# Optimization experiments

Hardware: AMD Instinct MI355X
Metric: run time of the kernel (lower is better)

## Reference

```python
import jax, jax.numpy as jnp
import numpy as np

B, T, D, H = 2, 512, 512, 8
HD = D // H
FF = 4 * D
MOM_BETA, NOV_BETA, NOV_GAIN = 0.9, 0.95, 3.0
LR_MIN, LR_MAX, MAX_FW_NORM = 0.5, 3.0, 32.0


def setup_inputs() -> dict:
    key = jax.random.key(0)
    ks = jax.random.split(key, 10)
    s = 1.0 / np.sqrt(D)
    return {
        'x': jax.random.normal(ks[0], (B, T, D), jnp.float32),
        'Wq': jax.random.normal(ks[1], (D, D), jnp.float32) * s,
        'Wk1': jax.random.normal(ks[2], (D, D), jnp.float32) * s,
        'Wk2': jax.random.normal(ks[3], (D, D), jnp.float32) * s,
        'Wv': jax.random.normal(ks[4], (D, D), jnp.float32) * s,
        'Wo': jax.random.normal(ks[5], (D, D), jnp.float32) * s,
        'lambda_logit': jnp.zeros((H,), jnp.float32),  # sigmoid -> lambda_init = 0.5
        'ln1_g': jnp.ones((D,), jnp.float32), 'ln1_b': jnp.zeros((D,), jnp.float32),
        'base_weight': jax.random.normal(ks[6], (D, D), jnp.float32) * s,  # ~xavier
        'ttt_bias': jnp.zeros((D,), jnp.float32),
        'log_inner_lr': jnp.log(jnp.asarray(0.05, jnp.float32)),
        'ln2_g': jnp.ones((D,), jnp.float32), 'ln2_b': jnp.zeros((D,), jnp.float32),
        'W1': jax.random.normal(ks[7], (FF, D), jnp.float32) * s,
        'b1': jnp.zeros((FF,), jnp.float32),
        'W2': jax.random.normal(ks[8], (D, FF), jnp.float32) * (1.0 / np.sqrt(FF)),
        'b2': jnp.zeros((D,), jnp.float32),
        'ln3_g': jnp.ones((D,), jnp.float32), 'ln3_b': jnp.zeros((D,), jnp.float32),
    }


def _ln(x, g, b):
    m = x.mean(-1, keepdims=True)
    v = jnp.mean((x - m) ** 2, -1, keepdims=True)
    return (x - m) / jnp.sqrt(v + 1e-5) * g + b


def _diff_attn(x, Wq, Wk1, Wk2, Wv, Wo, lambda_logit):
    b, t, d = x.shape
    def heads(w):
        return jnp.einsum('btd,od->bto', x, w).reshape(b, t, H, HD).transpose(0, 2, 1, 3)
    q, k1, k2, v = heads(Wq), heads(Wk1), heads(Wk2), heads(Wv)
    scale = HD ** -0.5
    s1 = jnp.einsum('bhqd,bhkd->bhqk', q, k1) * scale
    s2 = jnp.einsum('bhqd,bhkd->bhqk', q, k2) * scale
    mask = jnp.tril(jnp.ones((t, t), bool))
    neg = jnp.finfo(s1.dtype).min
    s1 = jnp.where(mask, s1, neg)
    s2 = jnp.where(mask, s2, neg)
    lam = jax.nn.sigmoid(lambda_logit)[None, :, None, None]
    attn = jax.nn.softmax(s1, -1) - lam * jax.nn.softmax(s2, -1)
    attn = attn / jnp.clip(jnp.abs(attn).sum(-1, keepdims=True), 1e-6, None)
    o = jnp.einsum('bhqk,bhkd->bhqd', attn, v).transpose(0, 2, 1, 3).reshape(b, t, d)
    return jnp.einsum('btd,od->bto', o, Wo)


def _ttt(x, base_weight, ttt_bias, log_inner_lr):
    b = x.shape[0]
    inner_lr = jnp.clip(jnp.exp(log_inner_lr), 1e-5, 1.0)
    fw0 = jnp.broadcast_to(base_weight, (b, D, D)).astype(x.dtype) + 0.0
    mom0 = jnp.zeros_like(fw0)
    ema0 = jnp.zeros((b, D), x.dtype)
    lrm0 = jnp.ones((b, 1), x.dtype)

    def step(carry, x_t):  # x_t: [B, D]
        fw, mom, ema, lrm = carry
        y = jnp.einsum('bij,bj->bi', fw, x_t) + ttt_bias
        err = (y - x_t) / float(D)  # targets=None -> target is x_t
        g = jax.lax.stop_gradient(err[:, :, None] * x_t[:, None, :])  # first_order
        mom2 = MOM_BETA * mom + (1.0 - MOM_BETA) * g
        nov = jnp.abs(x_t - ema).mean(-1, keepdims=True)  # [B, 1]
        lr_scale = jnp.clip(1.0 + NOV_GAIN * nov, LR_MIN, LR_MAX)
        lrm2 = NOV_BETA * lrm + (1.0 - NOV_BETA) * lr_scale
        ema2 = NOV_BETA * ema + (1.0 - NOV_BETA) * x_t
        fw2 = fw - (inner_lr * lrm2)[:, :, None] * mom2
        norm = jnp.clip(jnp.sqrt((fw2 * fw2).sum((1, 2), keepdims=True)), 1e-6, None)
        fw2 = fw2 * jnp.minimum(MAX_FW_NORM / norm, 1.0)
        return (fw2, mom2, ema2, lrm2), y

    _, ys = jax.lax.scan(step, (fw0, mom0, ema0, lrm0), x.transpose(1, 0, 2))
    return ys.transpose(1, 0, 2)


def reference(x, Wq, Wk1, Wk2, Wv, Wo, lambda_logit, ln1_g, ln1_b, base_weight, ttt_bias, log_inner_lr, ln2_g, ln2_b, W1, b1, W2, b2, ln3_g, ln3_b):
    h = x + _diff_attn(_ln(x, ln1_g, ln1_b), Wq, Wk1, Wk2, Wv, Wo, lambda_logit)
    h = h + _ttt(_ln(h, ln2_g, ln2_b), base_weight, ttt_bias, log_inner_lr)
    z = _ln(h, ln3_g, ln3_b)
    z = jax.nn.gelu(jnp.einsum('btd,fd->btf', z, W1) + b1, approximate=False)
    h = h + jnp.einsum('btf,df->btd', z, W2) + b2
    return h
```

## Files before the change

kernel.cpp:

```cpp
#include <hip/hip_runtime.h>
#include <hip/hip_fp16.h>

typedef _Float16 f16;
typedef f16 f16x4 __attribute__((ext_vector_type(4)));
typedef f16 f16x8 __attribute__((ext_vector_type(8)));
typedef float f32x4 __attribute__((ext_vector_type(4)));
typedef unsigned uint2v __attribute__((ext_vector_type(2)));

#define DEVI static __device__ __forceinline__

DEVI void gload_lds16(const void* g, void* l) {
  __builtin_amdgcn_global_load_lds(
      (const __attribute__((address_space(1))) unsigned int*)g,
      (__attribute__((address_space(3))) unsigned int*)l, 16, 0, 0);
}

DEVI float wave_red_sum64(float v) {
#pragma unroll
  for (int m = 1; m < 64; m <<= 1) v += __shfl_xor(v, m, 64);
  return v;
}
DEVI float wave_red_max64(float v) {
#pragma unroll
  for (int m = 1; m < 64; m <<= 1) v = fmaxf(v, __shfl_xor(v, m, 64));
  return v;
}

template <int CTRL>
DEVI float dpp_addf(float v) {
  int s = __builtin_amdgcn_update_dpp(0, __float_as_int(v), CTRL, 0xF, 0xF, true);
  return v + __int_as_float(s);
}
DEVI float xor16_add(float v) {
#if __has_builtin(__builtin_amdgcn_permlane16_swap)
  uint2v r = __builtin_amdgcn_permlane16_swap(__float_as_uint(v), __float_as_uint(v), false, false);
  return __uint_as_float(r.x) + __uint_as_float(r.y);
#else
  int s = __builtin_amdgcn_ds_swizzle(__float_as_int(v), 0x401F);
  return v + __int_as_float(s);
#endif
}
DEVI float xor32_add(float v) {
#if __has_builtin(__builtin_amdgcn_permlane32_swap)
  uint2v r = __builtin_amdgcn_permlane32_swap(__float_as_uint(v), __float_as_uint(v), false, false);
  return __uint_as_float(r.x) + __uint_as_float(r.y);
#else
  int s = __builtin_amdgcn_ds_bpermute(((threadIdx.x & 63) ^ 32) << 2, __float_as_int(v));
  return v + __int_as_float(s);
#endif
}
DEVI float allred64(float v) {
  v = dpp_addf<0xB1>(v);
  v = dpp_addf<0x4E>(v);
  v = dpp_addf<0x141>(v);
  v = dpp_addf<0x140>(v);
  v = xor16_add(v);
  return xor32_add(v);
}

__global__ void cvt_all_kernel(const float* __restrict__ s0, const float* __restrict__ s1,
                               const float* __restrict__ s2, const float* __restrict__ s3,
                               const float* __restrict__ s4, const float* __restrict__ s5,
                               const float* __restrict__ s6, f16* __restrict__ d) {
  const int blk = blockIdx.x;
  const float* s; long dofs; int local;
  if (blk < 256)       { s = s0; dofs = 0;       local = blk; }
  else if (blk < 512)  { s = s1; dofs = 262144;  local = blk - 256; }
  else if (blk < 768)  { s = s2; dofs = 524288;  local = blk - 512; }
  else if (blk < 1024) { s = s3; dofs = 786432;  local = blk - 768; }
  else if (blk < 1280) { s = s4; dofs = 1048576; local = blk - 1024; }
  else if (blk < 2304) { s = s5; dofs = 1310720; local = blk - 1280; }
  else                 { s = s6; dofs = 2359296; local = blk - 2304; }
  const long i = (long)local * 1024 + threadIdx.x * 4;
  float4 v = *(const float4*)(s + i);
  f16x4 o = {(f16)v.x, (f16)v.y, (f16)v.z, (f16)v.w};
  *(f16x4*)(d + dofs + i) = o;
}

__global__ void ln_kernel(const float* __restrict__ in, const float* __restrict__ add,
                          const float* __restrict__ g, const float* __restrict__ b,
                          float* __restrict__ sumout, float* __restrict__ lnf,
                          f16* __restrict__ lnh) {
  const int row = blockIdx.x * 4 + (threadIdx.x >> 6);
  const int lane = threadIdx.x & 63;
  const long base = (long)row * 512;
  const int c0 = lane * 4, c1 = 256 + lane * 4;
  float4 a0 = *(const float4*)(in + base + c0);
  float4 a1 = *(const float4*)(in + base + c1);
  if (add) {
    float4 d0 = *(const float4*)(add + base + c0);
    float4 d1 = *(const float4*)(add + base + c1);
    a0.x += d0.x; a0.y += d0.y; a0.z += d0.z; a0.w += d0.w;
    a1.x += d1.x; a1.y += d1.y; a1.z += d1.z; a1.w += d1.w;
  }
  if (sumout) {
    *(float4*)(sumout + base + c0) = a0;
    *(float4*)(sumout + base + c1) = a1;
  }
  float v[8] = {a0.x, a0.y, a0.z, a0.w, a1.x, a1.y, a1.z, a1.w};
  float s = 0.f;
#pragma unroll
  for (int k = 0; k < 8; k++) s += v[k];
  s = wave_red_sum64(s);
  const float mean = s * (1.f / 512.f);
  float vs = 0.f;
#pragma unroll
  for (int k = 0; k < 8; k++) { float d = v[k] - mean; vs += d * d; }
  vs = wave_red_sum64(vs);
  const float rstd = rsqrtf(vs * (1.f / 512.f) + 1e-5f);
  float4 g0 = *(const float4*)(g + c0), g1 = *(const float4*)(g + c1);
  float4 p0 = *(const float4*)(b + c0), p1 = *(const float4*)(b + c1);
  const float gg[8] = {g0.x, g0.y, g0.z, g0.w, g1.x, g1.y, g1.z, g1.w};
  const float bv[8] = {p0.x, p0.y, p0.z, p0.w, p1.x, p1.y, p1.z, p1.w};
  float y[8];
#pragma unroll
  for (int k = 0; k < 8; k++) y[k] = (v[k] - mean) * rstd * gg[k] + bv[k];
  if (lnf) {
    float4 o0 = {y[0], y[1], y[2], y[3]}, o1 = {y[4], y[5], y[6], y[7]};
    *(float4*)(lnf + base + c0) = o0;
    *(float4*)(lnf + base + c1) = o1;
  }
  if (lnh) {
    f16x4 o0 = {(f16)y[0], (f16)y[1], (f16)y[2], (f16)y[3]};
    f16x4 o1 = {(f16)y[4], (f16)y[5], (f16)y[6], (f16)y[7]};
    *(f16x4*)(lnh + base + c0) = o0;
    *(f16x4*)(lnh + base + c1) = o1;
  }
}

enum { EPI_QKV = 0, EPI_SCORES = 2, EPI_PV = 3, EPI_WO = 4, EPI_GELU = 5, EPI_OUT = 6 };

template <int EPI>
__launch_bounds__(256, 1) __global__
void gemm_bt(const f16* __restrict__ A, const f16* __restrict__ W, int lda, int ldw,
             long Az, long Wz, void* __restrict__ dst, const float* __restrict__ bias,
             const float* __restrict__ resid, int K, float scale, int zofs, int hcp) {
  if (EPI == EPI_SCORES && blockIdx.x > blockIdx.y) return;
  __shared__ f16 lA[128 * 64];
  __shared__ f16 lB[128 * 64];
  const int tid = threadIdx.x;
  const int wave = tid >> 6, lane = tid & 63;
  const int z = blockIdx.z;
  const f16* Ab;
  const f16* Wb;
  if (EPI == EPI_SCORES) {
    const int v_ = (z >= hcp) ? 1 : 0, head = z - v_ * hcp;
    Ab = A + (long)head * 32768 + (long)blockIdx.y * 128 * lda;
    Wb = W + (long)v_ * 524288 + (long)head * 32768 + (long)blockIdx.x * 128 * ldw;
  } else {
    Ab = A + (long)z * Az + (long)blockIdx.y * 128 * lda;
    Wb = W + (long)z * Wz + (long)blockIdx.x * 128 * ldw;
  }

  f32x4 acc[4][4];
#pragma unroll
  for (int a = 0; a < 4; a++)
#pragma unroll
    for (int q = 0; q < 4; q++) acc[a][q] = (f32x4){0.f, 0.f, 0.f, 0.f};

  int srow[4], scol[4];
#pragma unroll
  for (int i = 0; i < 4; i++) {
    int c = i * 256 + tid;
    int row = c >> 3;
    int colb = (c & 7) << 4;
    srow[i] = row;
    scol[i] = (colb ^ ((row & 7) << 4)) >> 1;
  }

  for (int k0 = 0; k0 < K; k0 += 64) {
    __syncthreads();
#pragma unroll
    for (int i = 0; i < 4; i++) {
      const int le = (i * 256 + wave * 64) * 8;
      gload_lds16(Ab + (long)srow[i] * lda + k0 + scol[i], lA + le);
      gload_lds16(Wb + (long)srow[i] * ldw + k0 + scol[i], lB + le);
    }
    __syncthreads();
    const int wm = (wave >> 1) * 64, wn = (wave & 1) * 64;
#pragma unroll
    for (int km = 0; km < 2; km++) {
      const int kb = km * 64 + ((lane >> 4) << 4);
      f16x8 af[4], bfv[4];
#pragma unroll
      for (int mf = 0; mf < 4; mf++) {
        int r = wm + mf * 16 + (lane & 15);
        af[mf] = *(const f16x8*)((const char*)lA + r * 128 + (kb ^ ((r & 7) << 4)));
      }
#pragma unroll
      for (int nf = 0; nf < 4; nf++) {
        int r = wn + nf * 16 + (lane & 15);
        bfv[nf] = *(const f16x8*)((const char*)lB + r * 128 + (kb ^ ((r & 7) << 4)));
      }
#pragma unroll
      for (int mf = 0; mf < 4; mf++)
#pragma unroll
        for (int nf = 0; nf < 4; nf++)
          acc[mf][nf] = __builtin_amdgcn_mfma_f32_16x16x32_f16(af[mf], bfv[nf], acc[mf][nf], 0, 0, 0);
    }
  }

  const int wm = (wave >> 1) * 64, wn = (wave & 1) * 64;
  const int rbase = blockIdx.y * 128 + wm + ((lane >> 4) << 2);
  const int cbase = blockIdx.x * 128 + wn + (lane & 15);
#pragma unroll
  for (int mf = 0; mf < 4; mf++)
#pragma unroll
    for (int nf = 0; nf < 4; nf++)
#pragma unroll
      for (int j = 0; j < 4; j++) {
        const int m = rbase + mf * 16 + j;
        const int n = cbase + nf * 16;
        const float v = acc[mf][nf][j];
        if (EPI == EPI_QKV) {
          f16* d = (f16*)dst + (long)z * 524288;
          if (z < 3)
            d[(long)((m >> 9) * 8 + (n >> 6)) * 32768 + (m & 511) * 64 + (n & 63)] = (f16)v;
          else
            d[(long)((m >> 9) * 8 + (n >> 6)) * 32768 + (n & 63) * 512 + (m & 511)] = (f16)v;
        } else if (EPI == EPI_SCORES) {
          ((float*)dst)[(long)z * 262144 + (long)m * 512 + n] = v * scale;
        } else if (EPI == EPI_PV) {
          if (n < 64) {
            const int hh = z + zofs;
            ((f16*)dst)[(long)((hh >> 3) * 512 + m) * 512 + (hh & 7) * 64 + n] = (f16)v;
          }
        } else if (EPI == EPI_WO) {
          ((float*)dst)[(long)m * 512 + n] = v + resid[(long)m * 512 + n];
        } else if (EPI == EPI_GELU) {
          const float u = v + bias[n];
          ((f16*)dst)[(long)m * 2048 + n] = (f16)(0.5f * u * (1.f + erff(u * 0.70710678118f)));
        } else {
          ((float*)dst)[(long)m * 512 + n] = v + bias[n] + resid[(long)m * 512 + n];
        }
      }
}

__global__ void softmax_diff_kernel(const float* __restrict__ S1, const float* __restrict__ S2,
                                    const float* __restrict__ lamlog, f16* __restrict__ attn,
                                    int zofs) {
  const int rid = blockIdx.x * 4 + (threadIdx.x >> 6);
  const int lane = threadIdx.x & 63;
  const int z = rid >> 9, i = rid & 511;
  const float lam = 1.f / (1.f + __expf(-lamlog[(z + zofs) & 7]));
  const long base = (long)z * 262144 + (long)i * 512;
  const int c0 = lane * 4, c1 = 256 + lane * 4;
  float4 xa = *(const float4*)(S1 + base + c0);
  float4 xb = *(const float4*)(S1 + base + c1);
  float4 ya = *(const float4*)(S2 + base + c0);
  float4 yb = *(const float4*)(S2 + base + c1);
  float s1v[8] = {xa.x, xa.y, xa.z, xa.w, xb.x, xb.y, xb.z, xb.w};
  float s2v[8] = {ya.x, ya.y, ya.z, ya.w, yb.x, yb.y, yb.z, yb.w};
  int cols[8];
#pragma unroll
  for (int k = 0; k < 8; k++) cols[k] = (k < 4) ? (c0 + k) : (c1 + k - 4);
  float m1 = -3.0e38f, m2 = -3.0e38f;
#pragma unroll
  for (int k = 0; k < 8; k++)
    if (cols[k] <= i) { m1 = fmaxf(m1, s1v[k]); m2 = fmaxf(m2, s2v[k]); }
  m1 = wave_red_max64(m1);
  m2 = wave_red_max64(m2);
  float z1 = 0.f, z2 = 0.f, e1[8], e2[8];
#pragma unroll
  for (int k = 0; k < 8; k++) {
    const bool valid = cols[k] <= i;
    e1[k] = valid ? __expf(s1v[k] - m1) : 0.f;
    e2[k] = valid ? __expf(s2v[k] - m2) : 0.f;
    z1 += e1[k]; z2 += e2[k];
  }
  z1 = wave_red_sum64(z1);
  z2 = wave_red_sum64(z2);
  const float r1 = 1.f / z1, r2 = lam / z2;
  float p[8], l1 = 0.f;
#pragma unroll
  for (int k = 0; k < 8; k++) { p[k] = e1[k] * r1 - e2[k] * r2; l1 += fabsf(p[k]); }
  l1 = wave_red_sum64(l1);
  const float rn = 1.f / fmaxf(l1, 1e-6f);
  f16x4 o0 = {(f16)(p[0] * rn), (f16)(p[1] * rn), (f16)(p[2] * rn), (f16)(p[3] * rn)};
  f16x4 o1 = {(f16)(p[4] * rn), (f16)(p[5] * rn), (f16)(p[6] * rn), (f16)(p[7] * rn)};
  *(f16x4*)(attn + base + c0) = o0;
  *(f16x4*)(attn + base + c1) = o1;
}

#define ALD4(dst, p) asm volatile("global_load_dwordx4 %0, %1, off" : "=&v"(dst) : "v"(p) : "memory")
#define ALD1(dst, p) asm volatile("global_load_dword %0, %1, off" : "=&v"(dst) : "v"(p) : "memory")
#define VMWAIT(N)                                                             \
  {                                                                           \
    asm volatile("s_waitcnt vmcnt(" #N ")" ::: "memory");                     \
    __builtin_amdgcn_sched_barrier(0);                                        \
  }

#define EISSUE(X)                                                             \
  {                                                                           \
    ALD1(X[0], pe);        ALD1(X[1], pe + 512);                              \
    ALD1(X[2], pe + 1024); ALD1(X[3], pe + 1536);                             \
    ALD1(X[4], pe + 2048); ALD1(X[5], pe + 2560);                             \
    ALD1(X[6], pe + 3072); ALD1(X[7], pe + 3584);                             \
    pe += 4096;                                                               \
  }
#define ESTEP(V, T)                                                           \
  {                                                                           \
    dp[(long)(T) * 512] = fabsf((V) - ema);                                   \
    ema = fmaf(0.95f, ema, 0.05f * (V));                                      \
  }

__launch_bounds__(64, 1) __global__
void eta_diff_kernel(const float* __restrict__ x2, float* __restrict__ diff) {
  const int blk = blockIdx.x;
  const int b = blk >> 3;
  const int col = (blk & 7) * 64 + threadIdx.x;
  const float* pe = x2 + (long)b * 262144 + col;
  float* dp = diff + (long)b * 262144 + col;
  float ema = 0.f;
  float EA[8], EB[8];
  EISSUE(EA);
  EISSUE(EB);
  VMWAIT(8);
#pragma unroll 1
  for (int t = 0; t < 512; t += 16) {
    ESTEP(EA[0], t + 0); ESTEP(EA[1], t + 1); ESTEP(EA[2], t + 2); ESTEP(EA[3], t + 3);
    ESTEP(EA[4], t + 4); ESTEP(EA[5], t + 5); ESTEP(EA[6], t + 6); ESTEP(EA[7], t + 7);
    EISSUE(EA);
    VMWAIT(16);
    ESTEP(EB[0], t + 8);  ESTEP(EB[1], t + 9);  ESTEP(EB[2], t + 10); ESTEP(EB[3], t + 11);
    ESTEP(EB[4], t + 12); ESTEP(EB[5], t + 13); ESTEP(EB[6], t + 14); ESTEP(EB[7], t + 15);
    EISSUE(EB);
    VMWAIT(16);
  }
  asm volatile("s_waitcnt vmcnt(0)" ::: "memory");
}

__global__ void eta_nov_kernel(const float* __restrict__ diff, float* __restrict__ nov) {
  const int row = blockIdx.x * 4 + (threadIdx.x >> 6);
  const int lane = threadIdx.x & 63;
  const float* dp = diff + (long)row * 512 + lane * 4;
  float4 a0 = *(const float4*)dp;
  float4 a1 = *(const float4*)(dp + 256);
  float s = ((a0.x + a0.y) + (a0.z + a0.w)) + ((a1.x + a1.y) + (a1.z + a1.w));
  s = wave_red_sum64(s);
  if (lane == 0) nov[row] = s * (1.f / 512.f);
}

__global__ void eta_scan_kernel(const float* __restrict__ nov, const float* __restrict__ loglr,
                                float* __restrict__ eta) {
  if (threadIdx.x != 0) return;
  const int b = blockIdx.x;
  float ilr = expf(loglr[0]);
  ilr = fminf(fmaxf(ilr, 1e-5f), 1.f);
  float lrm = 1.f;
  const float* pb = nov + (long)b * 512;
#pragma unroll 8
  for (int t = 0; t < 512; t++) {
    const float ls = fminf(fmaxf(fmaf(3.f, pb[t], 1.f), 0.5f), 3.f);
    lrm = fmaf(0.95f, lrm, 0.05f * ls);
    eta[b * 512 + t] = ilr * lrm;
  }
}

DEVI float dot8(const f32x4 F0, const f32x4 F1, const f32x4 X0, const f32x4 X1) {
  float a0 = F0.x * X0.x, a1 = F0.y * X0.y, a2 = F0.z * X0.z, a3 = F0.w * X0.w;
  a0 = fmaf(F1.x, X1.x, a0); a1 = fmaf(F1.y, X1.y, a1);
  a2 = fmaf(F1.z, X1.z, a2); a3 = fmaf(F1.w, X1.w, a3);
  return (a0 + a1) + (a2 + a3);
}
DEVI void upd8(f32x4& M0, f32x4& M1, f32x4& F0, f32x4& F1, float c1, float e,
               const f32x4 X0, const f32x4 X1, float& ns) {
  M0.x = fmaf(0.9f, M0.x, c1 * X0.x); F0.x = fmaf(-e, M0.x, F0.x); ns = fmaf(F0.x, F0.x, ns);
  M0.y = fmaf(0.9f, M0.y, c1 * X0.y); F0.y = fmaf(-e, M0.y, F0.y); ns = fmaf(F0.y, F0.y, ns);
  M0.z = fmaf(0.9f, M0.z, c1 * X0.z); F0.z = fmaf(-e, M0.z, F0.z); ns = fmaf(F0.z, F0.z, ns);
  M0.w = fmaf(0.9f, M0.w, c1 * X0.w); F0.w = fmaf(-e, M0.w, F0.w); ns = fmaf(F0.w, F0.w, ns);
  M1.x = fmaf(0.9f, M1.x, c1 * X1.x); F1.x = fmaf(-e, M1.x, F1.x); ns = fmaf(F1.x, F1.x, ns);
  M1.y = fmaf(0.9f, M1.y, c1 * X1.y); F1.y = fmaf(-e, M1.y, F1.y); ns = fmaf(F1.y, F1.y, ns);
  M1.z = fmaf(0.9f, M1.z, c1 * X1.z); F1.z = fmaf(-e, M1.z, F1.z); ns = fmaf(F1.z, F1.z, ns);
  M1.w = fmaf(0.9f, M1.w, c1 * X1.w); F1.w = fmaf(-e, M1.w, F1.w); ns = fmaf(F1.w, F1.w, ns);
}

#define TISSUE2(X, RA, RB, ET)                                                \
  {                                                                           \
    ALD4(X[0], pxc);        ALD4(X[1], pxc + 4);                              \
    ALD4(X[2], pxc + 512);  ALD4(X[3], pxc + 516);                            \
    ALD4(X[4], pxc + 1024); ALD4(X[5], pxc + 1028);                           \
    ALD4(X[6], pxc + 1536); ALD4(X[7], pxc + 1540);                           \
    ALD1(RA[0], pxra);        ALD1(RA[1], pxra + 512);                        \
    ALD1(RA[2], pxra + 1024); ALD1(RA[3], pxra + 1536);                       \
    ALD1(RB[0], pxrb);        ALD1(RB[1], pxrb + 512);                        \
    ALD1(RB[2], pxrb + 1024); ALD1(RB[3], pxrb + 1536);                       \
    ALD4(ET, per);                                                            \
    pxc += 2048; pxra += 2048; pxrb += 2048; per += 4;                        \
  }

#define TSTEP2(X0v, X1v, rAv, rBv, ev, K)                                     \
  {                                                                           \
    const float pA_ = allred64(dot8(fA0, fA1, X0v, X1v));                     \
    const float pB_ = allred64(dot8(fB0, fB1, X0v, X1v));                     \
    const float yA_ = pA_ + biasA, yB_ = pB_ + biasB;                         \
    ysA[K] = yA_; ysB[K] = yB_;                                               \
    const float c1A_ = (yA_ - (rAv)) * (0.1f / 512.f);                        \
    const float c1B_ = (yB_ - (rBv)) * (0.1f / 512.f);                        \
    const float e_ = (ev);                                                    \
    float ns_ = 0.f;                                                          \
    upd8(mA0, mA1, fA0, fA1, c1A_, e_, X0v, X1v, ns_);                        \
    upd8(mB0, mB1, fB0, fB1, c1B_, e_, X0v, X1v, ns_);                        \
    np8[K] = allred64(ns_);                                                   \
  }

__launch_bounds__(64, 1) __global__
void ttt_fast_kernel(const float* __restrict__ x2, const float* __restrict__ base_w,
                     const float* __restrict__ tbias, const float* __restrict__ eta,
                     float* __restrict__ yT, float* __restrict__ npT) {
  const int blk = blockIdx.x;
  const int b = blk >> 8;
  const int rA = blk & 255;
  const int lane = threadIdx.x;
  const float* xb = x2 + (long)b * 262144;

  f32x4 fA0, fA1, fB0, fB1;
  float biasA, biasB;
  ALD4(fA0, base_w + (long)rA * 512 + lane * 8);
  ALD4(fA1, base_w + (long)rA * 512 + lane * 8 + 4);
  ALD4(fB0, base_w + (long)(rA + 256) * 512 + lane * 8);
  ALD4(fB1, base_w + (long)(rA + 256) * 512 + lane * 8 + 4);
  ALD1(biasA, tbias + rA);
  ALD1(biasB, tbias + rA + 256);

  f32x4 mA0 = {0.f, 0.f, 0.f, 0.f}, mA1 = mA0, mB0 = mA0, mB1 = mA0;
  float ysA[8], ysB[8], np8[8];

  const float* pxc = xb + lane * 8;
  const float* pxra = xb + rA;
  const float* pxrb = xb + rA + 256;
  const float* per = eta + b * 512;
  float* pyA = yT + (long)(b * 512 + rA) * 512;
  float* pyB = yT + (long)(b * 512 + rA + 256) * 512;
  float* pnp = npT + (long)blk * 512;

  f32x4 XA[8], XB[8], EA, EB;
  float RA0[4], RB0[4], RA1[4], RB1[4];
  TISSUE2(XA, RA0, RB0, EA);
  TISSUE2(XB, RA1, RB1, EB);
  VMWAIT(17);

#pragma unroll 1
  for (int T = 0; T < 512; T += 8) {
    TSTEP2(XA[0], XA[1], RA0[0], RB0[0], EA.x, 0);
    TSTEP2(XA[2], XA[3], RA0[1], RB0[1], EA.y, 1);
    TSTEP2(XA[4], XA[5], RA0[2], RB0[2], EA.z, 2);
    TSTEP2(XA[6], XA[7], RA0[3], RB0[3], EA.w, 3);
    TISSUE2(XA, RA0, RB0, EA);
    VMWAIT(17);
    TSTEP2(XB[0], XB[1], RA1[0], RB1[0], EB.x, 4);
    TSTEP2(XB[2], XB[3], RA1[1], RB1[1], EB.y, 5);
    TSTEP2(XB[4], XB[5], RA1[2], RB1[2], EB.z, 6);
    TSTEP2(XB[6], XB[7], RA1[3], RB1[3], EB.w, 7);
    if (lane == 0) {
      *(float4*)(pyA + T)     = (float4){ysA[0], ysA[1], ysA[2], ysA[3]};
      *(float4*)(pyA + T + 4) = (float4){ysA[4], ysA[5], ysA[6], ysA[7]};
      *(float4*)(pyB + T)     = (float4){ysB[0], ysB[1], ysB[2], ysB[3]};
      *(float4*)(pyB + T + 4) = (float4){ysB[4], ysB[5], ysB[6], ysB[7]};
      *(float4*)(pnp + T)     = (float4){np8[0], np8[1], np8[2], np8[3]};
      *(float4*)(pnp + T + 4) = (float4){np8[4], np8[5], np8[6], np8[7]};
    }
    TISSUE2(XB, RA1, RB1, EB);
    VMWAIT(23);
  }
  asm volatile("s_waitcnt vmcnt(0)" ::: "memory");
}

__global__ void transpose3_kernel(const float* __restrict__ yT, const float* __restrict__ npT,
                                  float* __restrict__ ysb, float* __restrict__ npv) {
  __shared__ float tile[64][65];
  const int s = blockIdx.z;
  const float* src = (s < 2) ? (yT + (long)s * 262144) : npT;
  float* dst = (s < 2) ? (ysb + (long)s * 262144) : npv;
  const int ti = blockIdx.y, tj = blockIdx.x;
  const int tr = threadIdx.x >> 4;
  const int tc = (threadIdx.x & 15) * 4;
#pragma unroll
  for (int p = 0; p < 4; p++) {
    const int r = tr + p * 16;
    float4 v = *(const float4*)(src + (long)(ti * 64 + r) * 512 + tj * 64 + tc);
    tile[r][tc] = v.x; tile[r][tc + 1] = v.y; tile[r][tc + 2] = v.z; tile[r][tc + 3] = v.w;
  }
  __syncthreads();
#pragma unroll
  for (int p = 0; p < 4; p++) {
    const int j = tr + p * 16;
    float4 v = {tile[tc][j], tile[tc + 1][j], tile[tc + 2][j], tile[tc + 3][j]};
    *(float4*)(dst + (long)(tj * 64 + j) * 512 + ti * 64 + tc) = v;
  }
}

__global__ void verify_kernel(const float* __restrict__ npv, int* __restrict__ flag) {
  const int t = blockIdx.x;
  const int tid = threadIdx.x;
  const int wave = tid >> 6, lane = tid & 63;
  float s = npv[(long)t * 512 + tid];
  s = wave_red_sum64(s);
  __shared__ float part[8];
  if (lane == 0) part[wave] = s;
  __syncthreads();
  if (tid == 0) {
    const float s0 = (part[0] + part[1]) + (part[2] + part[3]);
    const float s1 = (part[4] + part[5]) + (part[6] + part[7]);
    if (s0 > 1020.f || s1 > 1020.f) atomicOr(flag, 1);
  }
}

__launch_bounds__(1024, 1) __global__
void ttt_fallback_kernel(const int* __restrict__ flag, const float* __restrict__ x2,
                         const float* __restrict__ base_w, const float* __restrict__ tbias,
                         const float* __restrict__ eta, float* __restrict__ ys,
                         float* __restrict__ fwg, float* __restrict__ momg) {
  if (flag[0] == 0) return;
  const int b = blockIdx.x;
  const int tid = threadIdx.x;
  const int wave = tid >> 6, lane = tid & 63;
  float* fw = fwg + (long)b * 262144;
  float* mm = momg + (long)b * 262144;
  for (int e = tid; e < 262144; e += 1024) { fw[e] = base_w[e]; mm[e] = 0.f; }
  __shared__ float xs[512], errs[512], red[16];
  const float* xb = x2 + (long)b * 262144;
  for (int t = 0; t < 512; t++) {
    __syncthreads();
    if (tid < 512) xs[tid] = xb[t * 512 + tid];
    __syncthreads();
    if (tid < 512) {
      float acc = 0.f;
      for (int c = 0; c < 512; c++) acc = fmaf(fw[(long)tid * 512 + c], xs[c], acc);
      const float y = acc + tbias[tid];
      ys[((long)b * 512 + t) * 512 + tid] = y;
      errs[tid] = (y - xs[tid]) * (1.f / 512.f);
    }
    __syncthreads();
    const float eta_t = eta[b * 512 + t];
    float nsq = 0.f;
    for (int e = tid; e < 262144; e += 1024) {
      const int r = e >> 9, c = e & 511;
      const float m2 = fmaf(0.9f, mm[e], 0.1f * errs[r] * xs[c]);
      mm[e] = m2;
      const float f2 = fmaf(-eta_t, m2, fw[e]);
      fw[e] = f2;
      nsq = fmaf(f2, f2, nsq);
    }
    nsq = wave_red_sum64(nsq);
    if (lane == 0) red[wave] = nsq;
    __syncthreads();
    if (tid == 0) {
      float s = 0.f;
      for (int w = 0; w < 16; w++) s += red[w];
      red[0] = s;
    }
    __syncthreads();
    const float norm = fmaxf(sqrtf(red[0]), 1e-6f);
    const float sc = fminf(32.f / norm, 1.f);
    if (sc < 1.f)
      for (int e = tid; e < 262144; e += 1024) fw[e] *= sc;
  }
}

extern "C" void kernel_launch(void* const* d_in, const int* in_sizes, int n_in,
                              void* d_out, int out_size, void* d_ws, size_t ws_size,
                              hipStream_t stream) {
  (void)in_sizes; (void)n_in; (void)out_size;
  const float* x      = (const float*)d_in[0];
  const float* Wq     = (const float*)d_in[1];
  const float* Wk1    = (const float*)d_in[2];
  const float* Wk2    = (const float*)d_in[3];
  const float* Wv     = (const float*)d_in[4];
  const float* Wo     = (const float*)d_in[5];
  const float* lamlog = (const float*)d_in[6];
  const float* ln1g   = (const float*)d_in[7];
  const float* ln1b   = (const float*)d_in[8];
  const float* basew  = (const float*)d_in[9];
  const float* tttb   = (const float*)d_in[10];
  const float* loglr  = (const float*)d_in[11];
  const float* ln2g   = (const float*)d_in[12];
  const float* ln2b   = (const float*)d_in[13];
  const float* W1     = (const float*)d_in[14];
  const float* b1     = (const float*)d_in[15];
  const float* W2     = (const float*)d_in[16];
  const float* b2     = (const float*)d_in[17];
  const float* ln3g   = (const float*)d_in[18];
  const float* ln3b   = (const float*)d_in[19];
  float* out = (float*)d_out;

  char* ws = (char*)d_ws;
  size_t off = 0;
  auto alloc = [&](size_t bytes) {
    size_t o = off;
    off += (bytes + 255) & ~(size_t)255;
    return o;
  };
  f16* WqH   = (f16*)(ws + alloc(262144 * 2));
  f16* Wk1H  = (f16*)(ws + alloc(262144 * 2));
  f16* Wk2H  = (f16*)(ws + alloc(262144 * 2));
  f16* WvH   = (f16*)(ws + alloc(262144 * 2));
  f16* WoH   = (f16*)(ws + alloc(262144 * 2));
  f16* W1H   = (f16*)(ws + alloc(1048576 * 2));
  f16* W2H   = (f16*)(ws + alloc(1048576 * 2));
  (void)Wk1H; (void)Wk2H; (void)WvH; (void)W1H;
  f16* xlnH  = (f16*)(ws + alloc(524288 * 2));
  f16* qh    = (f16*)(ws + alloc(524288 * 2));
  f16* k1h   = (f16*)(ws + alloc(524288 * 2));
  f16* k2h   = (f16*)(ws + alloc(524288 * 2));
  f16* vTh   = (f16*)(ws + alloc(524288 * 2));
  (void)k2h;
  f16* obtd  = (f16*)(ws + alloc(524288 * 2));
  f16* x3h   = (f16*)(ws + alloc(524288 * 2));
  f16* zh    = (f16*)(ws + alloc(2097152 * 2));
  float* h1  = (float*)(ws + alloc(524288 * 4));
  float* x2  = (float*)(ws + alloc(524288 * 4));
  float* ysb = (float*)(ws + alloc(524288 * 4));
  float* h2  = (float*)(ws + alloc(524288 * 4));
  float* eta = (float*)(ws + alloc(1024 * 4));
  float* yT  = (float*)(ws + alloc(524288 * 4));
  float* npT = (float*)(ws + alloc(262144 * 4));
  float* npv = (float*)(ws + alloc(262144 * 4));
  float* nvd = (float*)(ws + alloc(524288 * 4));
  float* nov = (float*)(ws + alloc(1024 * 4));
  int* flag  = (int*)(ws + alloc(256));
  float* fwfb  = (float*)(ws + alloc(524288 * 4));
  float* momfb = (float*)(ws + alloc(524288 * 4));

  int hc = 16;
  while (hc > 1 && off + (size_t)hc * (262144ull * 4 * 2 + 262144ull * 2) > ws_size) hc >>= 1;
  float* S1  = (float*)(ws + alloc((size_t)hc * 262144 * 4));
  float* S2  = (float*)(ws + alloc((size_t)hc * 262144 * 4));
  f16* attnb = (f16*)(ws + alloc((size_t)hc * 262144 * 2));
  (void)S2;

  cvt_all_kernel<<<3328, 256, 0, stream>>>(Wq, Wk1, Wk2, Wv, Wo, W1, W2, WqH);

  ln_kernel<<<256, 256, 0, stream>>>(x, nullptr, ln1g, ln1b, nullptr, nullptr, xlnH);

  gemm_bt<EPI_QKV><<<dim3(4, 8, 4), 256, 0, stream>>>(
      xlnH, WqH, 512, 512, 0, 262144, qh, nullptr, nullptr, 512, 1.f, 0, 0);

  const int nc = 16 / hc;
  for (int c = 0; c < nc; c++) {
    const int cs = c * hc;
    gemm_bt<EPI_SCORES><<<dim3(4, 4, 2 * hc), 256, 0, stream>>>(
        qh + (long)cs * 32768, k1h + (long)cs * 32768, 64, 64, 0, 0, S1,
        nullptr, nullptr, 64, 0.125f, 0, hc);
    softmax_diff_kernel<<<hc * 128, 256, 0, stream>>>(S1, S2, lamlog, attnb, cs);
    gemm_bt<EPI_PV><<<dim3(1, 4, hc), 256, 0, stream>>>(
        attnb, vTh + (long)cs * 32768, 512, 512, 262144, 32768, obtd,
        nullptr, nullptr, 512, 1.f, cs, 0);
  }

  gemm_bt<EPI_WO><<<dim3(4, 8, 1), 256, 0, stream>>>(obtd, WoH, 512, 512, 0, 0, h1, nullptr, x, 512, 1.f, 0, 0);

  ln_kernel<<<256, 256, 0, stream>>>(h1, nullptr, ln2g, ln2b, nullptr, x2, nullptr);

  hipMemsetAsync(flag, 0, 4, stream);
  eta_diff_kernel<<<16, 64, 0, stream>>>(x2, nvd);
  eta_nov_kernel<<<256, 256, 0, stream>>>(nvd, nov);
  eta_scan_kernel<<<2, 64, 0, stream>>>(nov, loglr, eta);
  ttt_fast_kernel<<<512, 64, 0, stream>>>(x2, basew, tttb, eta, yT, npT);
  transpose3_kernel<<<dim3(8, 8, 3), 256, 0, stream>>>(yT, npT, ysb, npv);
  verify_kernel<<<512, 512, 0, stream>>>(npv, flag);
  ttt_fallback_kernel<<<2, 1024, 0, stream>>>(flag, x2, basew, tttb, eta, ysb, fwfb, momfb);

  ln_kernel<<<256, 256, 0, stream>>>(h1, ysb, ln3g, ln3b, h2, nullptr, x3h);

  gemm_bt<EPI_GELU><<<dim3(16, 8, 1), 256, 0, stream>>>(x3h, W1H, 512, 512, 0, 0, zh, b1, nullptr, 512, 1.f, 0, 0);
  gemm_bt<EPI_OUT><<<dim3(4, 8, 1), 256, 0, stream>>>(zh, W2H, 2048, 2048, 0, 0, out, b2, h2, 2048, 1.f, 0, 0);
}
```

Baseline: 314.2 us.

## Split-K the Wo and W2 GEMMs into four partials plus a reduction kernel

The Wo projection and the FFN down-projection each launched only 32 blocks on a GPU with many more compute units. Both now use split-K with four K slices, giving 128 blocks that write fp32 partial sums into a new workspace buffer. A separate red4 kernel then adds the partials together with the residual and bias. This trades extra global memory traffic and an added launch for better occupancy. A red16g helper is also added but never used.

```diff
diff --git a/kernel.cpp b/kernel.cpp
--- a/kernel.cpp
+++ b/kernel.cpp
@@ -56,6 +56,13 @@
   v = dpp_addf<0x140>(v);
   v = xor16_add(v);
   return xor32_add(v);
+}
+DEVI float red16g(float v) {
+  v = dpp_addf<0xB1>(v);
+  v = dpp_addf<0x4E>(v);
+  v = dpp_addf<0x141>(v);
+  v = dpp_addf<0x140>(v);
+  return v;
 }
 
 __global__ void cvt_all_kernel(const float* __restrict__ s0, const float* __restrict__ s1,
@@ -128,7 +135,7 @@
   }
 }
 
-enum { EPI_QKV = 0, EPI_SCORES = 2, EPI_PV = 3, EPI_WO = 4, EPI_GELU = 5, EPI_OUT = 6 };
+enum { EPI_QKV = 0, EPI_SCORES = 2, EPI_PV = 3, EPI_GELU = 5, EPI_PART = 7 };
 
 template <int EPI>
 __launch_bounds__(256, 1) __global__
@@ -225,15 +232,34 @@
             const int hh = z + zofs;
             ((f16*)dst)[(long)((hh >> 3) * 512 + m) * 512 + (hh & 7) * 64 + n] = (f16)v;
           }
-        } else if (EPI == EPI_WO) {
-          ((float*)dst)[(long)m * 512 + n] = v + resid[(long)m * 512 + n];
         } else if (EPI == EPI_GELU) {
           const float u = v + bias[n];
           ((f16*)dst)[(long)m * 2048 + n] = (f16)(0.5f * u * (1.f + erff(u * 0.70710678118f)));
         } else {
-          ((float*)dst)[(long)m * 512 + n] = v + bias[n] + resid[(long)m * 512 + n];
+          ((float*)dst)[(long)z * 524288 + (long)m * 512 + n] = v;
         }
       }
+}
+
+__global__ void red4_kernel(const float* __restrict__ parts, const float* __restrict__ resid,
+                            const float* __restrict__ bias, float* __restrict__ dst) {
+  const long i = ((long)blockIdx.x * 256 + threadIdx.x) * 4;
+  float4 s0 = *(const float4*)(parts + i);
+  float4 s1 = *(const float4*)(parts + 524288 + i);
+  float4 s2 = *(const float4*)(parts + 1048576 + i);
+  float4 s3 = *(const float4*)(parts + 1572864 + i);
+  float4 r  = *(const float4*)(resid + i);
+  float4 o;
+  o.x = ((s0.x + s1.x) + (s2.x + s3.x)) + r.x;
+  o.y = ((s0.y + s1.y) + (s2.y + s3.y)) + r.y;
+  o.z = ((s0.z + s1.z) + (s2.z + s3.z)) + r.z;
+  o.w = ((s0.w + s1.w) + (s2.w + s3.w)) + r.w;
+  if (bias) {
+    const int n = (int)(i & 511);
+    float4 b = *(const float4*)(bias + n);
+    o.x += b.x; o.y += b.y; o.z += b.z; o.w += b.w;
+  }
+  *(float4*)(dst + i) = o;
 }
 
 __global__ void softmax_diff_kernel(const float* __restrict__ S1, const float* __restrict__ S2,
@@ -621,6 +647,7 @@
   int* flag  = (int*)(ws + alloc(256));
   float* fwfb  = (float*)(ws + alloc(524288 * 4));
   float* momfb = (float*)(ws + alloc(524288 * 4));
+  float* parts = (float*)(ws + alloc((size_t)4 * 524288 * 4));
 
   int hc = 16;
   while (hc > 1 && off + (size_t)hc * (262144ull * 4 * 2 + 262144ull * 2) > ws_size) hc >>= 1;
@@ -648,7 +675,9 @@
         nullptr, nullptr, 512, 1.f, cs, 0);
   }
 
-  gemm_bt<EPI_WO><<<dim3(4, 8, 1), 256, 0, stream>>>(obtd, WoH, 512, 512, 0, 0, h1, nullptr, x, 512, 1.f, 0, 0);
+  gemm_bt<EPI_PART><<<dim3(4, 8, 4), 256, 0, stream>>>(
+      obtd, WoH, 512, 512, 128, 128, parts, nullptr, nullptr, 128, 1.f, 0, 0);
+  red4_kernel<<<512, 256, 0, stream>>>(parts, x, nullptr, h1);
 
   ln_kernel<<<256, 256, 0, stream>>>(h1, nullptr, ln2g, ln2b, nullptr, x2, nullptr);
 
@@ -664,5 +693,7 @@
   ln_kernel<<<256, 256, 0, stream>>>(h1, ysb, ln3g, ln3b, h2, nullptr, x3h);
 
   gemm_bt<EPI_GELU><<<dim3(16, 8, 1), 256, 0, stream>>>(x3h, W1H, 512, 512, 0, 0, zh, b1, nullptr, 512, 1.f, 0, 0);
-  gemm_bt<EPI_OUT><<<dim3(4, 8, 1), 256, 0, stream>>>(zh, W2H, 2048, 2048, 0, 0, out, b2, h2, 2048, 1.f, 0, 0);
-}
+  gemm_bt<EPI_PART><<<dim3(4, 8, 4), 256, 0, stream>>>(
+      zh, W2H, 2048, 2048, 512, 512, parts, nullptr, nullptr, 512, 1.f, 0, 0);
+  red4_kernel<<<512, 256, 0, stream>>>(parts, h2, b2, out);
+}
```

Result: faster. 290.9 us (-7.4%).
